# Optimization experiments

Measured on AMD Instinct MI355X. Metric: run time of the kernel, lower is better.

Reference implementation:

```python
import jax, jax.numpy as jnp
import numpy as np

B, T, E, D, V = 64, 32, 512, 512, 32000


def setup_inputs() -> dict:
    key = jax.random.key(0)
    ks = jax.random.split(key, 7)
    encoder_out = jax.random.normal(ks[0], (B, T, E), jnp.float32)
    caption_lengths = jax.random.randint(ks[1], (B, 1), 2, T + 1, jnp.int32)
    caption_lengths = caption_lengths.at[0, 0].set(T)  # pin max length -> static pred shape
    s = 1.0 / np.sqrt(D).astype(np.float32)
    W_ih = jax.random.uniform(ks[2], (4 * D, E), jnp.float32, -s, s)
    W_hh = jax.random.uniform(ks[3], (4 * D, D), jnp.float32, -s, s)
    b_ih = jax.random.uniform(ks[4], (4 * D,), jnp.float32, -s, s)
    b_hh = jax.random.uniform(ks[5], (4 * D,), jnp.float32, -s, s)
    fc_w = jax.random.uniform(ks[6], (V, D), jnp.float32, -0.1, 0.1)  # reset_parameters
    fc_b = jnp.zeros((V,), jnp.float32)
    return {"encoder_out": encoder_out, "caption_lengths": caption_lengths,
            "W_ih": W_ih, "W_hh": W_hh, "b_ih": b_ih, "b_hh": b_hh,
            "fc_w": fc_w, "fc_b": fc_b}


def reference(encoder_out, caption_lengths, W_ih, W_hh, b_ih, b_hh, fc_w, fc_b):
    Bv, Tv, Ev = encoder_out.shape
    Dv = W_hh.shape[1]
    lens = caption_lengths[:, 0]
    sort_ind = jnp.argsort(-lens)          # descending sort, as in torch .sort(descending=True)
    dec_len = lens[sort_ind] - 1           # [B] decode_lengths
    enc = encoder_out[sort_ind]            # [B, T, E]
    h0 = jnp.zeros((Bv, Dv), encoder_out.dtype)

    # scan over timesteps 0..T-2 (max(decode_lengths) == T-1 by construction).
    # Shrinking-batch semantics (sorted desc) == freezing h,c of finished rows.
    xs = (jnp.arange(Tv - 1), jnp.swapaxes(enc[:, :Tv - 1], 0, 1))  # ([T-1], [T-1, B, E])

    def step(carry, inp):
        h, c = carry
        t, x = inp
        gates = x @ W_ih.T + b_ih + h @ W_hh.T + b_hh  # [B, 4D]
        i, f, g, o = jnp.split(gates, 4, axis=-1)
        i = jax.nn.sigmoid(i)
        f = jax.nn.sigmoid(f)
        g = jnp.tanh(g)
        o = jax.nn.sigmoid(o)
        c_new = f * c + i * g
        h_new = o * jnp.tanh(c_new)
        active = (t < dec_len)[:, None]                # [B, 1]
        h = jnp.where(active, h_new, h)
        c = jnp.where(active, c_new, c)
        preds = jnp.where(active, h_new @ fc_w.T + fc_b, 0.0)  # rows past batch_size_t stay 0
        return (h, c), preds

    (_, _), preds = jax.lax.scan(step, (h0, h0), xs)   # preds: [T-1, B, V]
    predictions = jnp.transpose(preds, (1, 0, 2))       # [B, T-1, V]
    return predictions, sort_ind
```

## Files before the change

### kernel.cpp

```cpp
#include <hip/hip_runtime.h>
#include <hip/hip_bf16.h>
#include <math.h>

#define B_  64
#define T_  32
#define E_  512
#define D_  512
#define V_  32000
#define NT  31
#define G4  2048
#define NBLK 256

typedef __attribute__((ext_vector_type(8))) short short8;
typedef __attribute__((ext_vector_type(4))) float f32x4;
typedef __hip_bfloat16 bf16;

__device__ __forceinline__ float sigmoidf_(float x) { return 1.f / (1.f + expf(-x)); }
__device__ __forceinline__ int perm_(int n) { return ((n & 3) << 9) + (n >> 2); }

__global__ void k_sort(const int* __restrict__ caplen, float* __restrict__ out_sind,
                       int* __restrict__ sind, int* __restrict__ declen,
                       int* __restrict__ Mact, int* __restrict__ rowlist,
                       float4* __restrict__ hz, int* __restrict__ cnt) {
    __shared__ int s_len[B_];
    __shared__ int s_dl[B_];
    __shared__ int s_cnt[NT];
    __shared__ int s_pre[NT + 1];
    int tid = threadIdx.x;
    if (tid < B_) s_len[tid] = caplen[tid];
    __syncthreads();
    if (tid < B_) {
        int len = s_len[tid];
        int rank = 0;
        for (int j = 0; j < B_; ++j) {
            int lj = s_len[j];
            rank += (lj > len) || (lj == len && j < tid);
        }
        sind[rank] = tid;
        declen[rank] = len - 1;
        s_dl[rank] = len - 1;
        out_sind[rank] = (float)tid;
    }
    __syncthreads();
    if (tid < NT) {
        int cntv = 0;
        for (int b = 0; b < B_; ++b) cntv += (tid < s_dl[b]);
        s_cnt[tid] = cntv;
    }
    __syncthreads();
    if (tid == 0) {
        int acc = 0;
        for (int t = 0; t < NT; ++t) { s_pre[t] = acc; acc += s_cnt[t]; }
        s_pre[NT] = acc;
        Mact[0] = acc;
    }
    __syncthreads();
    int Ma = s_pre[NT];
    for (int i = tid; i < NT * B_; i += blockDim.x) {
        int t = i >> 6, b = i & 63;
        bool act = (t < s_dl[b]);
        int pos = act ? (s_pre[t] + b)
                      : (Ma + (t * B_ - s_pre[t]) + (b - s_cnt[t]));
        rowlist[pos] = (t * B_ + b) | (act ? 0 : (1 << 30));
    }
    for (int i = tid; i < 8 * 16; i += blockDim.x) cnt[i] = 0;
    for (int i = tid; i < (2 * B_ * D_) / 4; i += blockDim.x)
        hz[i] = make_float4(0.f, 0.f, 0.f, 0.f);
}

__global__ __launch_bounds__(256) void k_xgemm(
    const float* __restrict__ enc, const float* __restrict__ Wih,
    const float* __restrict__ bih, const float* __restrict__ bhh,
    const int* __restrict__ sind, float* __restrict__ X) {
    __shared__ __align__(16) float sA[16 * 68];
    __shared__ __align__(16) float sB[16 * 68];
    __shared__ int s_sind[B_];
    int tid = threadIdx.x;
    int mt = blockIdx.x;
    int n0 = blockIdx.y * 64;
    if (tid < B_) s_sind[tid] = sind[tid];
    __syncthreads();
    int la = tid >> 2;
    int lk = (tid & 3) << 2;
    int tx = tid & 15, ty = tid >> 4;
    const float* arow = enc + ((long)s_sind[la] * T_ + mt) * E_;
    const float* brow = Wih + (long)perm_(n0 + la) * E_;
    float acc[4][4] = {};
    for (int k0 = 0; k0 < E_; k0 += 16) {
        float4 a4 = *(const float4*)(arow + k0 + lk);
        float4 b4 = *(const float4*)(brow + k0 + lk);
        sA[(lk + 0) * 68 + la] = a4.x; sA[(lk + 1) * 68 + la] = a4.y;
        sA[(lk + 2) * 68 + la] = a4.z; sA[(lk + 3) * 68 + la] = a4.w;
        sB[(lk + 0) * 68 + la] = b4.x; sB[(lk + 1) * 68 + la] = b4.y;
        sB[(lk + 2) * 68 + la] = b4.z; sB[(lk + 3) * 68 + la] = b4.w;
        __syncthreads();
        #pragma unroll
        for (int kk = 0; kk < 16; ++kk) {
            float4 av = *(const float4*)&sA[kk * 68 + (ty << 2)];
            float4 bv = *(const float4*)&sB[kk * 68 + (tx << 2)];
            float a[4] = { av.x, av.y, av.z, av.w };
            float b[4] = { bv.x, bv.y, bv.z, bv.w };
            #pragma unroll
            for (int i = 0; i < 4; ++i)
                #pragma unroll
                for (int j = 0; j < 4; ++j)
                    acc[i][j] = fmaf(a[i], b[j], acc[i][j]);
        }
        __syncthreads();
    }
    #pragma unroll
    for (int i = 0; i < 4; ++i) {
        int b = (ty << 2) + i;
        int row = mt * 64 + b;
        int col0 = n0 + (tx << 2);
        float* xp = X + (long)row * G4 + col0;
        #pragma unroll
        for (int j = 0; j < 4; ++j) {
            int pc = perm_(col0 + j);
            xp[j] = acc[i][j] + bih[pc] + bhh[pc];
        }
    }
}

__global__ __launch_bounds__(512) void k_lstm(
    const float* __restrict__ X, const float* __restrict__ Whh,
    float* __restrict__ hb0, float* __restrict__ hb1,
    bf16* __restrict__ hstoreb, const int* __restrict__ declen,
    int* __restrict__ cnt) {
    __shared__ __align__(16) float sW[8][520];
    __shared__ __align__(16) float sp[64 * 72];
    __shared__ float sg[8][65];
    __shared__ int sdl[B_];
    int tid = threadIdx.x;
    int bid = blockIdx.x;
    int n0 = bid * 8;
    if (tid < B_) sdl[tid] = declen[tid];
    {
        int ci = tid >> 6;
        int kb = (tid & 63) << 3;
        const float* wr = Whh + (long)perm_(n0 + ci) * D_ + kb;
        float4 w0 = *(const float4*)(wr + 0);
        float4 w1 = *(const float4*)(wr + 4);
        *(float4*)&sW[ci][kb + 0] = w0;
        *(float4*)&sW[ci][kb + 4] = w1;
    }
    __syncthreads();
    int tx = tid & 7;
    int ty = tid >> 3;
    int cb = tid & 63, cdl = (tid >> 6) & 1;
    int cd = bid * 2 + cdl;
    int cidx = cb * D_ + cd;
    float creg = 0.f;
    float hreg = 0.f;

    for (int t = 0; t < NT; ++t) {
        const float* hold = (t & 1) ? hb1 : hb0;
        float*       hnew = (t & 1) ? hb0 : hb1;
        const float* hrow = hold + ty * D_;
        float4 hv[16];
        #pragma unroll
        for (int kk = 0; kk < 16; ++kk) {
            const float* ap = hrow + ((tx + (kk << 3)) << 2);
            asm volatile("global_load_dwordx4 %0, %1, off sc0 sc1"
                         : "=v"(hv[kk]) : "v"(ap));
        }
        float xv = X[(t * B_ + ty) * G4 + (n0 + tx)];
        asm volatile("s_waitcnt vmcnt(0)" ::: "memory");
        __builtin_amdgcn_sched_barrier(0);
        float p[8] = {};
        #pragma unroll
        for (int kk = 0; kk < 16; ++kk) {
            int k = (tx + (kk << 3)) << 2;
            #pragma unroll
            for (int j = 0; j < 8; ++j) {
                float4 w4 = *(const float4*)&sW[j][k];
                p[j] = fmaf(hv[kk].x, w4.x, p[j]);
                p[j] = fmaf(hv[kk].y, w4.y, p[j]);
                p[j] = fmaf(hv[kk].z, w4.z, p[j]);
                p[j] = fmaf(hv[kk].w, w4.w, p[j]);
            }
        }
        float* spp = &sp[ty * 72 + tx * 8];
        *(float4*)(spp + 0) = make_float4(p[0], p[1], p[2], p[3]);
        *(float4*)(spp + 4) = make_float4(p[4], p[5], p[6], p[7]);
        __syncthreads();
        {
            float s = xv;
            #pragma unroll
            for (int q = 0; q < 8; ++q) s += sp[ty * 72 + q * 8 + tx];
            sg[tx][ty] = ((tx & 3) == 2) ? tanhf(s) : sigmoidf_(s);
        }
        __syncthreads();
        if (tid < 128) {
            float gi = sg[cdl * 4 + 0][cb];
            float gf = sg[cdl * 4 + 1][cb];
            float gg = sg[cdl * 4 + 2][cb];
            float go = sg[cdl * 4 + 3][cb];
            float cn = gf * creg + gi * gg;
            float hn = go * tanhf(cn);
            hstoreb[(t * B_ + cb) * D_ + cd] = __float2bfloat16(hn);
            if (t < sdl[cb]) { creg = cn; hreg = hn; }
            __hip_atomic_store((unsigned*)(hnew + cidx), __float_as_uint(hreg),
                               __ATOMIC_RELAXED, __HIP_MEMORY_SCOPE_AGENT);
        }
        if (t == NT - 1) break;
        __syncthreads();
        if (tid == 0)
            __hip_atomic_fetch_add(&cnt[(bid & 7) * 16], 1, __ATOMIC_RELAXED,
                                   __HIP_MEMORY_SCOPE_AGENT);
        if (tid < 8) {
            int target = (t + 1) * (NBLK / 8);
            while (__hip_atomic_load(&cnt[tid * 16], __ATOMIC_RELAXED,
                                     __HIP_MEMORY_SCOPE_AGENT) < target)
                __builtin_amdgcn_s_sleep(1);
        }
        __syncthreads();
    }
}

__global__ __launch_bounds__(256) void k_fc(
    const bf16* __restrict__ hstoreb, const float* __restrict__ fcw,
    const float* __restrict__ fcb, const int* __restrict__ rowlist,
    const int* __restrict__ Mact, float* __restrict__ out) {
    __shared__ ushort sB[64 * 512];
    int tid = threadIdx.x, lane = tid & 63, w = tid >> 6;
    int nb = blockIdx.x;
    int n0 = nb * 64;
    int Ma = Mact[0];
    {
        int ko = tid & 63;
        int c0 = tid >> 6;
        for (int c = c0; c < 64; c += 4) {
            const float* src = fcw + (long)(n0 + c) * D_ + ko * 8;
            float4 v0 = *(const float4*)(src + 0);
            float4 v1 = *(const float4*)(src + 4);
            short8 o;
            bf16 b0 = __float2bfloat16(v0.x), b1 = __float2bfloat16(v0.y);
            bf16 b2 = __float2bfloat16(v0.z), b3 = __float2bfloat16(v0.w);
            bf16 b4 = __float2bfloat16(v1.x), b5 = __float2bfloat16(v1.y);
            bf16 b6 = __float2bfloat16(v1.z), b7 = __float2bfloat16(v1.w);
            o[0] = *(short*)&b0; o[1] = *(short*)&b1; o[2] = *(short*)&b2; o[3] = *(short*)&b3;
            o[4] = *(short*)&b4; o[5] = *(short*)&b5; o[6] = *(short*)&b6; o[7] = *(short*)&b7;
            int phys = c * 1024 + ((ko * 16) ^ ((c & 7) << 4));
            *(short8*)((char*)sB + phys) = o;
        }
    }
    __syncthreads();
    int kq = lane >> 4;
    int sxor = (lane & 7) << 4;
    int kq16 = kq << 4;
    int sBase[4];
    #pragma unroll
    for (int ns = 0; ns < 4; ++ns) sBase[ns] = (ns * 16 + (lane & 15)) * 1024;
    float fq[4];
    #pragma unroll
    for (int ns = 0; ns < 4; ++ns) fq[ns] = fcb[n0 + ns * 16 + (lane & 15)];
    for (int rc = 0; rc < 16; ++rc) {
        int base = rc * 128 + w * 32 + (lane & 31);
        int rvec = (base < NT * B_) ? rowlist[base] : -1;
        f32x4 acc[2][4] = {};
        bool domfma = (rc * 128) < Ma;
        if (domfma) {
            const bf16* ap[2];
            #pragma unroll
            for (int ms = 0; ms < 2; ++ms) {
                int rv = __shfl(rvec, ms * 16 + (lane & 15), 64);
                int ra = (rv < 0) ? 0 : (rv & 2047);
                ap[ms] = hstoreb + (long)ra * D_ + kq * 8;
            }
            #pragma unroll 4
            for (int kci = 0; kci < 16; ++kci) {
                short8 a0 = *(const short8*)(ap[0] + kci * 32);
                short8 a1 = *(const short8*)(ap[1] + kci * 32);
                short8 b[4];
                #pragma unroll
                for (int ns = 0; ns < 4; ++ns)
                    b[ns] = *(const short8*)((const char*)sB + sBase[ns]
                                             + ((kci * 64 + kq16) ^ sxor));
                #pragma unroll
                for (int ns = 0; ns < 4; ++ns) {
                    acc[0][ns] = __builtin_amdgcn_mfma_f32_16x16x32_bf16(a0, b[ns], acc[0][ns], 0, 0, 0);
                    acc[1][ns] = __builtin_amdgcn_mfma_f32_16x16x32_bf16(a1, b[ns], acc[1][ns], 0, 0, 0);
                }
            }
        }
        #pragma unroll
        for (int ms = 0; ms < 2; ++ms) {
            #pragma unroll
            for (int r = 0; r < 4; ++r) {
                int rv = __shfl(rvec, ms * 16 + kq * 4 + r, 64);
                if (rv < 0) continue;
                bool act = !(rv & (1 << 30));
                int row = rv & 2047;
                int tt = row >> 6, b = row & 63;
                float* po = out + ((long)(b * NT + tt)) * V_ + n0 + (lane & 15);
                #pragma unroll
                for (int ns = 0; ns < 4; ++ns)
                    po[ns * 16] = act ? (acc[ms][ns][r] + fq[ns]) : 0.f;
            }
        }
    }
}

extern "C" void kernel_launch(void* const* d_in, const int* in_sizes, int n_in,
                              void* d_out, int out_size, void* d_ws, size_t ws_size,
                              hipStream_t stream) {
    const float* enc    = (const float*)d_in[0];
    const int*   caplen = (const int*)d_in[1];
    const float* Wih    = (const float*)d_in[2];
    const float* Whh    = (const float*)d_in[3];
    const float* bih    = (const float*)d_in[4];
    const float* bhh    = (const float*)d_in[5];
    const float* fcw    = (const float*)d_in[6];
    const float* fcb    = (const float*)d_in[7];
    float* out = (float*)d_out;

    char* ws = (char*)d_ws;
    int* sind    = (int*)ws;
    int* declen  = sind + 64;
    int* Mact    = declen + 64;
    int* rowlist = Mact + 64;
    int* cnt     = rowlist + 2048;
    char* p = (char*)(cnt + 8 * 16);
    p = (char*)(((size_t)p + 255) & ~(size_t)255);
    float* X      = (float*)p;            p += (size_t)NT * B_ * G4 * 4;
    float* h0     = (float*)p;            p += (size_t)B_ * D_ * 4;
    float* h1     = (float*)p;            p += (size_t)B_ * D_ * 4;
    bf16* hstoreb = (bf16*)p;             p += (size_t)NT * B_ * D_ * 2;

    float* out_sind = out + (long)B_ * NT * V_;

    k_sort<<<1, 256, 0, stream>>>(caplen, out_sind, sind, declen, Mact, rowlist,
                                  (float4*)h0, cnt);
    k_xgemm<<<dim3(NT, G4 / 64), 256, 0, stream>>>(enc, Wih, bih, bhh, sind, X);
    k_lstm<<<NBLK, 512, 0, stream>>>(X, Whh, h0, h1, hstoreb, declen, cnt);
    k_fc<<<dim3(V_ / 64), 256, 0, stream>>>(hstoreb, fcw, fcb, rowlist, Mact, out);
}
```

Before: 727.2 us.

## Retile LSTM recurrence into 2D batch-by-gate blocks and widen FC blocks

The recurrent kernel now assigns each block 32 gate columns by 16 batch rows instead of 8 columns by all 64 rows. Each thread computes 2 rows by 8 columns with a 16-way k split. This cuts the hidden-state bytes each block reloads per step while raising the W_hh slice held in shared memory. The grid barrier counters grow from 8 to 32 stripes. The FC kernel moves to 512 threads with 8 waves, each handling 16 rows instead of 32, which gives more parallelism per block at the cost of more shared-memory reads of the B tile per row.

```diff
diff --git a/kernel.cpp b/kernel.cpp
--- a/kernel.cpp
+++ b/kernel.cpp
@@ -63,7 +63,7 @@
                       : (Ma + (t * B_ - s_pre[t]) + (b - s_cnt[t]));
         rowlist[pos] = (t * B_ + b) | (act ? 0 : (1 << 30));
     }
-    for (int i = tid; i < 8 * 16; i += blockDim.x) cnt[i] = 0;
+    for (int i = tid; i < 32 * 16; i += blockDim.x) cnt[i] = 0;
     for (int i = tid; i < (2 * B_ * D_) / 4; i += blockDim.x)
         hz[i] = make_float4(0.f, 0.f, 0.f, 0.f);
 }
@@ -127,89 +127,100 @@
     float* __restrict__ hb0, float* __restrict__ hb1,
     bf16* __restrict__ hstoreb, const int* __restrict__ declen,
     int* __restrict__ cnt) {
-    __shared__ __align__(16) float sW[8][520];
-    __shared__ __align__(16) float sp[64 * 72];
-    __shared__ float sg[8][65];
-    __shared__ int sdl[B_];
+    __shared__ __align__(16) float sW[32 * 528];
+    __shared__ float sp[512 * 17];
+    __shared__ float sg[32 * 17];
     int tid = threadIdx.x;
     int bid = blockIdx.x;
-    int n0 = bid * 8;
-    if (tid < B_) sdl[tid] = declen[tid];
+    int cg = bid >> 2, rg = bid & 3;
+    int n0 = cg * 32;
+    int d0 = cg * 8;
+    int r0 = rg * 16;
     {
-        int ci = tid >> 6;
-        int kb = (tid & 63) << 3;
-        const float* wr = Whh + (long)perm_(n0 + ci) * D_ + kb;
-        float4 w0 = *(const float4*)(wr + 0);
-        float4 w1 = *(const float4*)(wr + 4);
-        *(float4*)&sW[ci][kb + 0] = w0;
-        *(float4*)&sW[ci][kb + 4] = w1;
-    }
-    __syncthreads();
-    int tx = tid & 7;
-    int ty = tid >> 3;
-    int cb = tid & 63, cdl = (tid >> 6) & 1;
-    int cd = bid * 2 + cdl;
-    int cidx = cb * D_ + cd;
+        int ci = tid & 31;
+        int kseg = tid >> 5;
+        const float* wr = Whh + (long)perm_(n0 + ci) * D_ + kseg * 32;
+        float* dst = &sW[ci * 528 + kseg * 32];
+        #pragma unroll
+        for (int i = 0; i < 8; ++i)
+            *(float4*)(dst + i * 4) = *(const float4*)(wr + i * 4);
+    }
+    int kq = tid & 15;
+    int rp = (tid >> 4) & 7;
+    int jo = tid >> 7;
+    int crow = tid >> 5;
+    int ccol = tid & 31;
+    int bl = tid & 15, dl = (tid >> 4) & 7;
+    int gb = r0 + bl;
+    int gd = d0 + dl;
+    int dlen = declen[gb];
     float creg = 0.f;
     float hreg = 0.f;
+    __syncthreads();
 
     for (int t = 0; t < NT; ++t) {
         const float* hold = (t & 1) ? hb1 : hb0;
         float*       hnew = (t & 1) ? hb0 : hb1;
-        const float* hrow = hold + ty * D_;
-        float4 hv[16];
-        #pragma unroll
-        for (int kk = 0; kk < 16; ++kk) {
-            const float* ap = hrow + ((tx + (kk << 3)) << 2);
-            asm volatile("global_load_dwordx4 %0, %1, off sc0 sc1"
-                         : "=v"(hv[kk]) : "v"(ap));
-        }
-        float xv = X[(t * B_ + ty) * G4 + (n0 + tx)];
+        float4 hv[2][8];
+        #pragma unroll
+        for (int kk = 0; kk < 8; ++kk) {
+            #pragma unroll
+            for (int dr = 0; dr < 2; ++dr) {
+                const float* ap = hold + (r0 + rp * 2 + dr) * D_ + kk * 64 + kq * 4;
+                asm volatile("global_load_dwordx4 %0, %1, off sc0 sc1"
+                             : "=v"(hv[dr][kk]) : "v"(ap));
+            }
+        }
+        float xv = X[(t * B_ + r0 + crow) * G4 + n0 + ccol];
         asm volatile("s_waitcnt vmcnt(0)" ::: "memory");
         __builtin_amdgcn_sched_barrier(0);
-        float p[8] = {};
-        #pragma unroll
-        for (int kk = 0; kk < 16; ++kk) {
-            int k = (tx + (kk << 3)) << 2;
+        float acc[2][8] = {};
+        #pragma unroll
+        for (int kk = 0; kk < 8; ++kk) {
+            float4 h0 = hv[0][kk];
+            float4 h1 = hv[1][kk];
             #pragma unroll
             for (int j = 0; j < 8; ++j) {
-                float4 w4 = *(const float4*)&sW[j][k];
-                p[j] = fmaf(hv[kk].x, w4.x, p[j]);
-                p[j] = fmaf(hv[kk].y, w4.y, p[j]);
-                p[j] = fmaf(hv[kk].z, w4.z, p[j]);
-                p[j] = fmaf(hv[kk].w, w4.w, p[j]);
+                float4 w4 = *(const float4*)&sW[(jo * 8 + j) * 528 + kk * 64 + kq * 4];
+                acc[0][j] = fmaf(h0.x, w4.x, acc[0][j]); acc[0][j] = fmaf(h0.y, w4.y, acc[0][j]);
+                acc[0][j] = fmaf(h0.z, w4.z, acc[0][j]); acc[0][j] = fmaf(h0.w, w4.w, acc[0][j]);
+                acc[1][j] = fmaf(h1.x, w4.x, acc[1][j]); acc[1][j] = fmaf(h1.y, w4.y, acc[1][j]);
+                acc[1][j] = fmaf(h1.z, w4.z, acc[1][j]); acc[1][j] = fmaf(h1.w, w4.w, acc[1][j]);
             }
         }
-        float* spp = &sp[ty * 72 + tx * 8];
-        *(float4*)(spp + 0) = make_float4(p[0], p[1], p[2], p[3]);
-        *(float4*)(spp + 4) = make_float4(p[4], p[5], p[6], p[7]);
+        #pragma unroll
+        for (int dr = 0; dr < 2; ++dr)
+            #pragma unroll
+            for (int j = 0; j < 8; ++j)
+                sp[((rp * 2 + dr) * 32 + jo * 8 + j) * 17 + kq] = acc[dr][j];
         __syncthreads();
         {
             float s = xv;
-            #pragma unroll
-            for (int q = 0; q < 8; ++q) s += sp[ty * 72 + q * 8 + tx];
-            sg[tx][ty] = ((tx & 3) == 2) ? tanhf(s) : sigmoidf_(s);
+            const float* spr = &sp[(crow * 32 + ccol) * 17];
+            #pragma unroll
+            for (int q = 0; q < 16; ++q) s += spr[q];
+            sg[ccol * 17 + crow] = ((ccol & 3) == 2) ? tanhf(s) : sigmoidf_(s);
         }
         __syncthreads();
         if (tid < 128) {
-            float gi = sg[cdl * 4 + 0][cb];
-            float gf = sg[cdl * 4 + 1][cb];
-            float gg = sg[cdl * 4 + 2][cb];
-            float go = sg[cdl * 4 + 3][cb];
+            float gi = sg[(dl * 4 + 0) * 17 + bl];
+            float gf = sg[(dl * 4 + 1) * 17 + bl];
+            float gg = sg[(dl * 4 + 2) * 17 + bl];
+            float go = sg[(dl * 4 + 3) * 17 + bl];
             float cn = gf * creg + gi * gg;
             float hn = go * tanhf(cn);
-            hstoreb[(t * B_ + cb) * D_ + cd] = __float2bfloat16(hn);
-            if (t < sdl[cb]) { creg = cn; hreg = hn; }
-            __hip_atomic_store((unsigned*)(hnew + cidx), __float_as_uint(hreg),
+            hstoreb[(t * B_ + gb) * D_ + gd] = __float2bfloat16(hn);
+            if (t < dlen) { creg = cn; hreg = hn; }
+            __hip_atomic_store((unsigned*)(hnew + gb * D_ + gd), __float_as_uint(hreg),
                                __ATOMIC_RELAXED, __HIP_MEMORY_SCOPE_AGENT);
         }
         if (t == NT - 1) break;
         __syncthreads();
         if (tid == 0)
-            __hip_atomic_fetch_add(&cnt[(bid & 7) * 16], 1, __ATOMIC_RELAXED,
+            __hip_atomic_fetch_add(&cnt[(bid & 31) * 16], 1, __ATOMIC_RELAXED,
                                    __HIP_MEMORY_SCOPE_AGENT);
-        if (tid < 8) {
-            int target = (t + 1) * (NBLK / 8);
+        if (tid < 32) {
+            int target = (t + 1) * (NBLK / 32);
             while (__hip_atomic_load(&cnt[tid * 16], __ATOMIC_RELAXED,
                                      __HIP_MEMORY_SCOPE_AGENT) < target)
                 __builtin_amdgcn_s_sleep(1);
@@ -218,7 +229,7 @@
     }
 }
 
-__global__ __launch_bounds__(256) void k_fc(
+__global__ __launch_bounds__(512) void k_fc(
     const bf16* __restrict__ hstoreb, const float* __restrict__ fcw,
     const float* __restrict__ fcb, const int* __restrict__ rowlist,
     const int* __restrict__ Mact, float* __restrict__ out) {
@@ -228,9 +239,8 @@
     int n0 = nb * 64;
     int Ma = Mact[0];
     {
-        int ko = tid & 63;
-        int c0 = tid >> 6;
-        for (int c = c0; c < 64; c += 4) {
+        int ko = lane;
+        for (int c = w; c < 64; c += 8) {
             const float* src = fcw + (long)(n0 + c) * D_ + ko * 8;
             float4 v0 = *(const float4*)(src + 0);
             float4 v1 = *(const float4*)(src + 4);
@@ -256,48 +266,37 @@
     #pragma unroll
     for (int ns = 0; ns < 4; ++ns) fq[ns] = fcb[n0 + ns * 16 + (lane & 15)];
     for (int rc = 0; rc < 16; ++rc) {
-        int base = rc * 128 + w * 32 + (lane & 31);
-        int rvec = (base < NT * B_) ? rowlist[base] : -1;
-        f32x4 acc[2][4] = {};
-        bool domfma = (rc * 128) < Ma;
+        int base = rc * 128 + w * 16;
+        int ridx = base + (lane & 15);
+        int rvec = (ridx < NT * B_) ? rowlist[ridx] : -1;
+        f32x4 acc[4] = {};
+        bool domfma = (base < Ma);
         if (domfma) {
-            const bf16* ap[2];
-            #pragma unroll
-            for (int ms = 0; ms < 2; ++ms) {
-                int rv = __shfl(rvec, ms * 16 + (lane & 15), 64);
-                int ra = (rv < 0) ? 0 : (rv & 2047);
-                ap[ms] = hstoreb + (long)ra * D_ + kq * 8;
-            }
+            const bf16* ap = hstoreb + (long)((rvec < 0) ? 0 : (rvec & 2047)) * D_ + kq * 8;
             #pragma unroll 4
             for (int kci = 0; kci < 16; ++kci) {
-                short8 a0 = *(const short8*)(ap[0] + kci * 32);
-                short8 a1 = *(const short8*)(ap[1] + kci * 32);
+                short8 a0 = *(const short8*)(ap + kci * 32);
                 short8 b[4];
                 #pragma unroll
                 for (int ns = 0; ns < 4; ++ns)
                     b[ns] = *(const short8*)((const char*)sB + sBase[ns]
                                              + ((kci * 64 + kq16) ^ sxor));
                 #pragma unroll
-                for (int ns = 0; ns < 4; ++ns) {
-                    acc[0][ns] = __builtin_amdgcn_mfma_f32_16x16x32_bf16(a0, b[ns], acc[0][ns], 0, 0, 0);
-                    acc[1][ns] = __builtin_amdgcn_mfma_f32_16x16x32_bf16(a1, b[ns], acc[1][ns], 0, 0, 0);
-                }
+                for (int ns = 0; ns < 4; ++ns)
+                    acc[ns] = __builtin_amdgcn_mfma_f32_16x16x32_bf16(a0, b[ns], acc[ns], 0, 0, 0);
             }
         }
         #pragma unroll
-        for (int ms = 0; ms < 2; ++ms) {
-            #pragma unroll
-            for (int r = 0; r < 4; ++r) {
-                int rv = __shfl(rvec, ms * 16 + kq * 4 + r, 64);
-                if (rv < 0) continue;
-                bool act = !(rv & (1 << 30));
-                int row = rv & 2047;
-                int tt = row >> 6, b = row & 63;
-                float* po = out + ((long)(b * NT + tt)) * V_ + n0 + (lane & 15);
-                #pragma unroll
-                for (int ns = 0; ns < 4; ++ns)
-                    po[ns * 16] = act ? (acc[ms][ns][r] + fq[ns]) : 0.f;
-            }
+        for (int r = 0; r < 4; ++r) {
+            int rv = __shfl(rvec, kq * 4 + r, 16);
+            if (rv < 0) continue;
+            bool act = !(rv & (1 << 30));
+            int row = rv & 2047;
+            int tt = row >> 6, b = row & 63;
+            float* po = out + ((long)(b * NT + tt)) * V_ + n0 + (lane & 15);
+            #pragma unroll
+            for (int ns = 0; ns < 4; ++ns)
+                po[ns * 16] = act ? (acc[ns][r] + fq[ns]) : 0.f;
         }
     }
 }
@@ -321,7 +320,7 @@
     int* Mact    = declen + 64;
     int* rowlist = Mact + 64;
     int* cnt     = rowlist + 2048;
-    char* p = (char*)(cnt + 8 * 16);
+    char* p = (char*)(cnt + 32 * 16);
     p = (char*)(((size_t)p + 255) & ~(size_t)255);
     float* X      = (float*)p;            p += (size_t)NT * B_ * G4 * 4;
     float* h0     = (float*)p;            p += (size_t)B_ * D_ * 4;
@@ -334,5 +333,5 @@
                                   (float4*)h0, cnt);
     k_xgemm<<<dim3(NT, G4 / 64), 256, 0, stream>>>(enc, Wih, bih, bhh, sind, X);
     k_lstm<<<NBLK, 512, 0, stream>>>(X, Whh, h0, h1, hstoreb, declen, cnt);
-    k_fc<<<dim3(V_ / 64), 256, 0, stream>>>(hstoreb, fcw, fcb, rowlist, Mact, out);
-}
+    k_fc<<<dim3(V_ / 64), 512, 0, stream>>>(hstoreb, fcw, fcb, rowlist, Mact, out);
+}
```

Result: faster. 645.1 us (-11.3%).
